# Kernel optimization log

Measured on AMD Instinct MI355X. Metric: run time of the kernel, lower is better.

Reference implementation:

```python
import jax, jax.numpy as jnp
import numpy as np

B, S, EMB, H = 4, 1024, 1024, 16
HD = EMB // H          # head_dim = 64
MAXP = 512             # RelativePositionalEncoder default max_position


def setup_inputs() -> dict:
    key = jax.random.key(0)
    ks = jax.random.split(key, 13)
    s = 1.0 / np.sqrt(EMB)  # xavier-ish scale keeps softmax logits sane
    return {
        "query": jax.random.normal(ks[0], (B, S, EMB), jnp.float32),
        "key": jax.random.normal(ks[1], (B, S, EMB), jnp.float32),
        "value": jax.random.normal(ks[2], (B, S, EMB), jnp.float32),
        "Wq": jax.random.normal(ks[3], (EMB, EMB), jnp.float32) * s,
        "bq": jnp.zeros((EMB,), jnp.float32),
        "Wk": jax.random.normal(ks[4], (EMB, EMB), jnp.float32) * s,
        "bk": jnp.zeros((EMB,), jnp.float32),
        "Wv": jax.random.normal(ks[5], (EMB, EMB), jnp.float32) * s,
        "bv": jnp.zeros((EMB,), jnp.float32),
        "Wo": jax.random.normal(ks[6], (EMB, EMB), jnp.float32) * s,
        "bo": jnp.zeros((EMB,), jnp.float32),
        "rel_k": jax.random.normal(ks[7], (2 * MAXP + 1, HD), jnp.float32) * 0.05,
        "rel_v": jax.random.normal(ks[8], (2 * MAXP + 1, HD), jnp.float32) * 0.05,
    }


def _split_heads(x):
    # [B,S,E] -> [B,S,H,HD] -> [B,H,S,HD] -> [B*H,S,HD]
    return x.reshape(B, S, H, HD).transpose(0, 2, 1, 3).reshape(B * H, S, HD)


def reference(query, key, value, Wq, bq, Wk, bk, Wv, bv, Wo, bo, rel_k, rel_v):
    scale = jnp.sqrt(jnp.asarray(HD, query.dtype))
    q = _split_heads(query @ Wq + bq)
    k = _split_heads(key @ Wk + bk)
    v = _split_heads(value @ Wv + bv)
    # relative position lookup tables: [Sq, Sk, HD]
    rp = jnp.clip(jnp.arange(S)[None, :] - jnp.arange(S)[:, None], -MAXP, MAXP) + MAXP
    a_key = rel_k[rp]
    a_value = rel_v[rp]
    qk = jnp.einsum('bqd,bkd->bqk', q, k)              # [B*H,S,S]
    rel_qk = jnp.einsum('bqd,qkd->bqk', q, a_key)      # relative score term
    attn = jax.nn.softmax((qk + rel_qk) / scale, axis=-1)
    out = jnp.einsum('bqk,bkd->bqd', attn, v) + jnp.einsum('bqk,qkd->bqd', attn, a_value)
    # faithful to original's view(num_heads, batch, -1, head_dim) then concat reshape
    out = out.reshape(H, B, S, HD).transpose(0, 2, 1, 3).reshape(B, S, H * HD)
    out = out @ Wo + bo
    return (out, attn)
```

## Files before the change

kernel.cpp:

```cpp
#include <hip/hip_runtime.h>


using s16x8 = __attribute__((ext_vector_type(8))) short;
using f32x4 = __attribute__((ext_vector_type(4))) float;

#define MFMA16 __builtin_amdgcn_mfma_f32_16x16x32_bf16

__device__ __forceinline__ float bf2f(unsigned short u) {
  union { unsigned int u; float f; } v; v.u = ((unsigned int)u) << 16; return v.f;
}
__device__ __forceinline__ unsigned short f2bf(float f) {
  union { float f; unsigned int u; } v; v.f = f;
  unsigned int r = (v.u + 0x7FFFu + ((v.u >> 16) & 1u)) >> 16;
  return (unsigned short)r;
}

__global__ void k_cvt_bf16(const float* __restrict__ in, unsigned short* __restrict__ out, int n) {
  int i = (blockIdx.x * 256 + threadIdx.x) * 8;
  if (i >= n) return;
  float4 a = *(const float4*)(in + i);
  float4 b = *(const float4*)(in + i + 4);
  s16x8 o;
  o[0] = (short)f2bf(a.x); o[1] = (short)f2bf(a.y); o[2] = (short)f2bf(a.z); o[3] = (short)f2bf(a.w);
  o[4] = (short)f2bf(b.x); o[5] = (short)f2bf(b.y); o[6] = (short)f2bf(b.z); o[7] = (short)f2bf(b.w);
  *(s16x8*)(out + i) = o;
}

__global__ void k_tr1024(const float* __restrict__ W, unsigned short* __restrict__ Wt) {
  __shared__ float t[32][33];
  int tx = threadIdx.x, ty = threadIdx.y;
  int n0 = blockIdx.x * 32, k0 = blockIdx.y * 32;
#pragma unroll
  for (int r = 0; r < 4; ++r)
    t[ty * 4 + r][tx] = W[(size_t)(k0 + ty * 4 + r) * 1024 + n0 + tx];
  __syncthreads();
#pragma unroll
  for (int r = 0; r < 4; ++r)
    Wt[(size_t)(n0 + ty * 4 + r) * 1024 + k0 + tx] = f2bf(t[tx][ty * 4 + r]);
}

__global__ void k_relprep(const float* __restrict__ rk, const float* __restrict__ rv,
                          unsigned short* __restrict__ relkb, unsigned short* __restrict__ rvTb) {
  int b = blockIdx.x;
  if (b < 33) {
    int i = (b * 256 + threadIdx.x) * 8;
    if (i < 65600) {
      float4 a = *(const float4*)(rk + i);
      float4 c = *(const float4*)(rk + i + 4);
      s16x8 o;
      o[0] = (short)f2bf(a.x); o[1] = (short)f2bf(a.y); o[2] = (short)f2bf(a.z); o[3] = (short)f2bf(a.w);
      o[4] = (short)f2bf(c.x); o[5] = (short)f2bf(c.y); o[6] = (short)f2bf(c.z); o[7] = (short)f2bf(c.w);
      *(s16x8*)(relkb + i) = o;
    }
  } else {
    int i = (b - 33) * 256 + threadIdx.x;
    if (i < 65600) {
      int p = i >> 6, d = i & 63;
      rvTb[d * 1040 + p] = f2bf(rv[i]);
    }
  }
}

__global__ __launch_bounds__(256)
void k_trV(const unsigned short* __restrict__ v, unsigned short* __restrict__ vt) {
  __shared__ unsigned short T[64][72];
  const int tid = threadIdx.x;
  const int bh = blockIdx.x >> 4;
  const int s0 = (blockIdx.x & 15) << 6;
  const int r = tid >> 2, cb = (tid & 3) << 4;
  const unsigned short* src = v + ((size_t)bh << 16) + (size_t)(s0 + r) * 64 + cb;
  *(s16x8*)&T[r][cb] = *(const s16x8*)src;
  *(s16x8*)&T[r][cb + 8] = *(const s16x8*)(src + 8);
  __syncthreads();
  unsigned short* dst = vt + ((size_t)bh << 16) + (size_t)r * 1024 + s0 + cb;
  s16x8 o0, o1;
#pragma unroll
  for (int e = 0; e < 8; ++e) o0[e] = T[cb + e][r];
#pragma unroll
  for (int e = 0; e < 8; ++e) o1[e] = T[cb + 8 + e][r];
  *(s16x8*)dst = o0;
  *(s16x8*)(dst + 8) = o1;
}

template <int MODE>
__global__ __launch_bounds__(256, 2)
void k_gemm(const unsigned short* __restrict__ A, const unsigned short* __restrict__ BT,
            const float* __restrict__ bias, void* __restrict__ Cout) {
  __shared__ alignas(16) unsigned short aT[2][4096];
  __shared__ alignas(16) unsigned short bT[2][2048];
  const int tid = threadIdx.x;
  const int lane = tid & 63;
  const int l15 = lane & 15, lhi = lane >> 4;
  const int w = tid >> 6;
  const int wr = w * 32;
  const int brow = blockIdx.y * 128, bcol = blockIdx.x * 64;
  f32x4 acc[2][4] = {};

#define STAGE(buf, kt) do {                                                              \
    int k0s = (kt) * 32;                                                                 \
    {                                                                                    \
      int c = tid;                                                                       \
      int row = c >> 2, k8 = (c & 3) * 8;                                                \
      __builtin_amdgcn_global_load_lds(                                                  \
        (const __attribute__((address_space(1))) void*)(A + (size_t)(brow + row) * 1024 + k0s + k8), \
        (__attribute__((address_space(3))) void*)(&aT[buf][c * 8]), 16, 0, 0);           \
      __builtin_amdgcn_global_load_lds(                                                  \
        (const __attribute__((address_space(1))) void*)(BT + (size_t)(bcol + row) * 1024 + k0s + k8),\
        (__attribute__((address_space(3))) void*)(&bT[buf][c * 8]), 16, 0, 0);           \
    }                                                                                    \
    {                                                                                    \
      int c = tid + 256;                                                                 \
      int row = c >> 2, k8 = (c & 3) * 8;                                                \
      __builtin_amdgcn_global_load_lds(                                                  \
        (const __attribute__((address_space(1))) void*)(A + (size_t)(brow + row) * 1024 + k0s + k8), \
        (__attribute__((address_space(3))) void*)(&aT[buf][c * 8]), 16, 0, 0);           \
    }                                                                                    \
  } while (0)

  int cur = 0;
  STAGE(0, 0);
  for (int kt = 0; kt < 32; ++kt) {
    __syncthreads();
    if (kt + 1 < 32) STAGE(cur ^ 1, kt + 1);
    s16x8 af[2], bfv[4];
#pragma unroll
    for (int m = 0; m < 2; ++m)
      af[m] = *(const s16x8*)&aT[cur][(wr + m * 16 + l15) * 32 + lhi * 8];
#pragma unroll
    for (int n = 0; n < 4; ++n)
      bfv[n] = *(const s16x8*)&bT[cur][(n * 16 + l15) * 32 + lhi * 8];
#pragma unroll
    for (int m = 0; m < 2; ++m)
#pragma unroll
      for (int n = 0; n < 4; ++n)
        acc[m][n] = MFMA16(af[m], bfv[n], acc[m][n], 0, 0, 0);
    __syncthreads();
    cur ^= 1;
  }
#undef STAGE

#pragma unroll
  for (int m = 0; m < 2; ++m) {
#pragma unroll
    for (int n = 0; n < 4; ++n) {
      int col = bcol + n * 16 + l15;
      float bs = bias[col];
#pragma unroll
      for (int j = 0; j < 4; ++j) {
        int r = brow + wr + m * 16 + lhi * 4 + j;
        float v = acc[m][n][j] + bs;
        if (MODE == 0) {
          int b = r >> 10, s = r & 1023, h = col >> 6, d = col & 63;
          ((unsigned short*)Cout)[(((size_t)((b << 4) + h) * 1024 + s) << 6) + d] = f2bf(v);
        } else {
          ((float*)Cout)[(size_t)r * 1024 + col] = v;
        }
      }
    }
  }
}

#define RPW 1032
#define PWP 520

__global__ __launch_bounds__(256, 3)
void k_attn(const unsigned short* __restrict__ qb, const unsigned short* __restrict__ kbm,
            const unsigned short* __restrict__ vT, const unsigned short* __restrict__ relk,
            const unsigned short* __restrict__ rvT, float* __restrict__ attn_out,
            unsigned short* __restrict__ xscr) {
  __shared__ alignas(16) unsigned short pbuf[16 * RPW];
  __shared__ alignas(16) unsigned short TbPw[16 * PWP];
  __shared__ float red[4][16];
  __shared__ float izS[16], plS[16], phS[16];
  __shared__ unsigned short bndS[32];

  const int tid = threadIdx.x;
  const int lane = tid & 63;
  const int w = tid >> 6;
  const int l15 = lane & 15, lhi = lane >> 4;
  const int orig = ((blockIdx.x & 7) << 9) | (blockIdx.x >> 3);
  const int bh = orig >> 6;
  const int q0 = (orig & 63) << 4;

  const unsigned short* Qh = qb + ((size_t)bh << 16);
  const unsigned short* Kh = kbm + ((size_t)bh << 16);
  const unsigned short* Vth = vT + ((size_t)bh << 16);

  const unsigned short* qp = Qh + (size_t)(q0 + l15) * 64 + lhi * 8;
  s16x8 qa0 = *(const s16x8*)qp;
  s16x8 qa1 = *(const s16x8*)(qp + 32);

  {
    int sel = (l15 == 1) ? 1024 : 0;
    const unsigned short* rp = relk + (size_t)sel * 64 + lhi * 8;
    s16x8 rb0 = *(const s16x8*)rp;
    s16x8 rb1 = *(const s16x8*)(rp + 32);
    f32x4 d = {0.f, 0.f, 0.f, 0.f};
    d = MFMA16(qa0, rb0, d, 0, 0, 0);
    d = MFMA16(qa1, rb1, d, 0, 0, 0);
    if (l15 < 2) {
#pragma unroll
      for (int j = 0; j < 4; ++j) bndS[l15 * 16 + lhi * 4 + j] = f2bf(d[j]);
    }
  }

  float zp = 0.f;
  for (int half = 0; half < 2; ++half) {
    const int khalf = half << 9;
    __syncthreads();

    for (int i = tid; i < 16 * 64; i += 256) {
      int row = i >> 6, c8 = (i & 63) << 3;
      int fl = q0 + row - khalf - 512;
      unsigned short vlo = bndS[row], vhi = bndS[16 + row];
      s16x8 o;
#pragma unroll
      for (int e = 0; e < 8; ++e) o[e] = (short)((c8 + e < fl) ? vlo : vhi);
      *(s16x8*)&TbPw[row * PWP + c8] = o;
    }
    __syncthreads();

    {
      int pmin = khalf - q0 + 497;
      int PT0 = (pmin < 0 ? 0 : pmin) & ~15;
      int PT1 = khalf - q0 + 1023; if (PT1 > 1024) PT1 = 1024;
      for (int pt = PT0 + w * 16; pt <= PT1; pt += 64) {
        int pr = pt + l15; if (pr > 1024) pr = 1024;
        const unsigned short* rp = relk + (size_t)pr * 64 + lhi * 8;
        s16x8 rf0 = *(const s16x8*)rp;
        s16x8 rf1 = *(const s16x8*)(rp + 32);
        f32x4 d = {0.f, 0.f, 0.f, 0.f};
        d = MFMA16(qa0, rf0, d, 0, 0, 0);
        d = MFMA16(qa1, rf1, d, 0, 0, 0);
#pragma unroll
        for (int j = 0; j < 4; ++j) {
          int qi = lhi * 4 + j;
          int p = pt + l15;
          int u = p - khalf + q0 + qi - 512;
          if (p <= 1024 && u >= 0 && u < 512) TbPw[qi * PWP + u] = f2bf(d[j]);
        }
      }
    }
    __syncthreads();

    for (int n = 0; n < 8; ++n) {
      const int ktile = khalf + w * 16 + n * 64;
      const unsigned short* kp = Kh + (size_t)(ktile + l15) * 64 + lhi * 8;
      s16x8 kf0 = *(const s16x8*)kp;
      s16x8 kf1 = *(const s16x8*)(kp + 32);
      f32x4 c = {0.f, 0.f, 0.f, 0.f};
      __builtin_amdgcn_s_setprio(1);
      c = MFMA16(kf0, qa0, c, 0, 0, 0);
      c = MFMA16(kf1, qa1, c, 0, 0, 0);
      __builtin_amdgcn_s_setprio(0);
      uint2 tv = *(const uint2*)&TbPw[l15 * PWP + (ktile - khalf) + lhi * 4];
      float t0 = bf2f((unsigned short)(tv.x & 0xFFFF));
      float t1 = bf2f((unsigned short)(tv.x >> 16));
      float t2 = bf2f((unsigned short)(tv.y & 0xFFFF));
      float t3 = bf2f((unsigned short)(tv.y >> 16));
      float e0 = __expf((c[0] + t0) * 0.125f);
      float e1 = __expf((c[1] + t1) * 0.125f);
      float e2 = __expf((c[2] + t2) * 0.125f);
      float e3 = __expf((c[3] + t3) * 0.125f);
      zp += (e0 + e1) + (e2 + e3);
      uint2 pk;
      pk.x = (unsigned int)f2bf(e0) | ((unsigned int)f2bf(e1) << 16);
      pk.y = (unsigned int)f2bf(e2) | ((unsigned int)f2bf(e3) << 16);
      *(uint2*)&pbuf[l15 * RPW + ktile + lhi * 4] = pk;
    }
  }

  zp += __shfl_xor(zp, 16, 64);
  zp += __shfl_xor(zp, 32, 64);
  if (lane < 16) red[w][lane] = zp;
  __syncthreads();
  if (tid < 16)
    izS[tid] = 1.0f / (red[0][tid] + red[1][tid] + red[2][tid] + red[3][tid]);

  {
    const int qi = tid >> 4, tq = tid & 15;
    const int qa = q0 + qi;
    int lo, hi;
    const bool isPh = (qa < 512);
    if (isPh) { lo = qa + 512; hi = 1024; }
    else      { lo = 0;        hi = qa - 511; }
    float s = 0.f;
    const unsigned short* srow = pbuf + qi * RPW;
    const int kb0 = lo & ~7;
    for (int k8 = kb0 + tq * 8; k8 < hi; k8 += 128) {
      s16x8 v8 = *(const s16x8*)&srow[k8];
#pragma unroll
      for (int e = 0; e < 8; ++e) {
        int k = k8 + e;
        s += (k >= lo && k < hi) ? bf2f((unsigned short)v8[e]) : 0.f;
      }
    }
#pragma unroll
    for (int off = 1; off < 16; off <<= 1) s += __shfl_xor(s, off, 64);
    if (tq == 0) { plS[qi] = isPh ? 0.f : s; phS[qi] = isPh ? s : 0.f; }
  }
  __syncthreads();

  {
    float* ao = attn_out + ((size_t)bh << 20) + ((size_t)q0 << 10);
#pragma unroll
    for (int n = 0; n < 8; ++n) {
      int row = (tid >> 7) + n * 2;
      int c8 = (tid & 127) << 3;
      float iz = izS[row];
      s16x8 p8 = *(const s16x8*)&pbuf[row * RPW + c8];
      f32x4 o0, o1;
      o0[0] = bf2f((unsigned short)p8[0]) * iz; o0[1] = bf2f((unsigned short)p8[1]) * iz;
      o0[2] = bf2f((unsigned short)p8[2]) * iz; o0[3] = bf2f((unsigned short)p8[3]) * iz;
      o1[0] = bf2f((unsigned short)p8[4]) * iz; o1[1] = bf2f((unsigned short)p8[5]) * iz;
      o1[2] = bf2f((unsigned short)p8[6]) * iz; o1[3] = bf2f((unsigned short)p8[7]) * iz;
      __builtin_nontemporal_store(o0, (f32x4*)(ao + (row << 10) + c8));
      __builtin_nontemporal_store(o1, (f32x4*)(ao + (row << 10) + c8 + 4));
    }
  }

  f32x4 acc = {0.f, 0.f, 0.f, 0.f};
  const int d0w = w << 4;
  const unsigned short* vrow = Vth + (size_t)(d0w + l15) * 1024 + lhi * 8;
#pragma unroll 8
  for (int kc = 0; kc < 1024; kc += 32) {
    s16x8 pa = *(const s16x8*)&pbuf[l15 * RPW + kc + lhi * 8];
    s16x8 vf = *(const s16x8*)(vrow + kc);
    acc = MFMA16(pa, vf, acc, 0, 0, 0);
  }

  const unsigned short* rrow = rvT + (size_t)(d0w + l15) * 1040 + lhi * 8;
  {
    const int sqi = tid >> 4, stq = tid & 15;
    const int ssh = sqi & 7, shs = ssh >> 1;
    const bool sodd = (ssh & 1) != 0;
    unsigned short* drow = TbPw + sqi * PWP;
    const unsigned short* srow = pbuf + sqi * RPW;
    for (int ph = 0; ph < 2; ++ph) {
      __syncthreads();
      const int base = q0 + sqi + (ph ? 0 : -512);
      for (int t = stq; t < 64; t += 16) {
        const int kw0 = base + t * 8;
        s16x8 o;
        if (kw0 >= 0 && kw0 + 8 <= 1024) {
          const int A = kw0 - ssh;
          union { s16x8 v; unsigned int u[4]; } a0, a1, ov;
          a0.v = *(const s16x8*)&srow[A];
          a1.v = *(const s16x8*)&srow[A + 8];
          unsigned int wd[8];
#pragma unroll
          for (int j2 = 0; j2 < 4; ++j2) { wd[j2] = a0.u[j2]; wd[4 + j2] = a1.u[j2]; }
          unsigned int v7[7];
#pragma unroll
          for (int j2 = 0; j2 < 7; ++j2) {
            unsigned int sf = (wd[j2] >> 16) | (wd[j2 + 1] << 16);
            v7[j2] = sodd ? sf : wd[j2];
          }
#pragma unroll
          for (int j2 = 0; j2 < 4; ++j2) {
            unsigned int t0 = (shs & 1) ? v7[j2 + 1] : v7[j2];
            unsigned int t1 = (shs & 1) ? v7[j2 + 3] : v7[j2 + 2];
            ov.u[j2] = (shs & 2) ? t1 : t0;
          }
          o = ov.v;
        } else if (kw0 + 8 <= 0 || kw0 >= 1024) {
          o = (s16x8){0, 0, 0, 0, 0, 0, 0, 0};
        } else {
#pragma unroll
          for (int e = 0; e < 8; ++e) {
            int k = kw0 + e;
            int kc2 = k < 0 ? 0 : (k > 1023 ? 1023 : k);
            unsigned short vv = srow[kc2];
            o[e] = (k >= 0 && k < 1024) ? (short)vv : (short)0;
          }
        }
        *(s16x8*)&drow[t * 8] = o;
        if (ph == 0 && t == 0) drow[0] = f2bf(plS[sqi]);
      }
      __syncthreads();
#pragma unroll 8
      for (int kc = 0; kc < 512; kc += 32) {
        s16x8 pa = *(const s16x8*)&TbPw[l15 * PWP + kc + lhi * 8];
        s16x8 rb = *(const s16x8*)(rrow + (ph << 9) + kc);
        acc = MFMA16(pa, rb, acc, 0, 0, 0);
      }
    }
  }

  float rv1024 = bf2f(rvT[(size_t)(d0w + l15) * 1040 + 1024]);
  const size_t fb = ((size_t)(bh >> 2) << 18) + ((size_t)(bh & 3) << 6);
#pragma unroll
  for (int j = 0; j < 4; ++j) {
    int qi = lhi * 4 + j;
    float v = (acc[j] + phS[qi] * rv1024) * izS[qi];
    xscr[fb + ((size_t)(q0 + qi) << 8) + d0w + l15] = f2bf(v);
  }
}

extern "C" void kernel_launch(void* const* d_in, const int* in_sizes, int n_in,
                              void* d_out, int out_size, void* d_ws, size_t ws_size,
                              hipStream_t stream) {
  (void)in_sizes; (void)n_in; (void)out_size; (void)ws_size;
  const float* query = (const float*)d_in[0];
  const float* key   = (const float*)d_in[1];
  const float* value = (const float*)d_in[2];
  const float* Wq = (const float*)d_in[3];
  const float* bq = (const float*)d_in[4];
  const float* Wk = (const float*)d_in[5];
  const float* bk = (const float*)d_in[6];
  const float* Wv = (const float*)d_in[7];
  const float* bv = (const float*)d_in[8];
  const float* Wo = (const float*)d_in[9];
  const float* bo = (const float*)d_in[10];
  const float* rel_k = (const float*)d_in[11];
  const float* rel_v = (const float*)d_in[12];

  char* ws = (char*)d_ws;
  const size_t MB = 1024 * 1024;
  unsigned short* qb    = (unsigned short*)(ws);
  unsigned short* kbuf  = (unsigned short*)(ws + 8 * MB);
  unsigned short* vbuf  = (unsigned short*)(ws + 16 * MB);
  unsigned short* tmp16 = (unsigned short*)(ws + 24 * MB);
  unsigned short* wt    = (unsigned short*)(ws + 32 * MB);
  unsigned short* relkb = (unsigned short*)(ws + 34 * MB);
  unsigned short* rvTb  = (unsigned short*)(ws + 34 * MB + 512 * 1024);
  unsigned short* vTb   = tmp16;
  unsigned short* xscr  = vbuf;

  float* out0 = (float*)d_out;
  float* attn_out = out0 + 4194304;

  dim3 trb(32, 8), trg(32, 32);
  dim3 gg(16, 32);

  k_relprep<<<290, 256, 0, stream>>>(rel_k, rel_v, relkb, rvTb);

  k_cvt_bf16<<<2048, 256, 0, stream>>>(query, tmp16, 4194304);
  k_tr1024<<<trg, trb, 0, stream>>>(Wq, wt);
  k_gemm<0><<<gg, 256, 0, stream>>>(tmp16, wt, bq, qb);

  k_cvt_bf16<<<2048, 256, 0, stream>>>(key, tmp16, 4194304);
  k_tr1024<<<trg, trb, 0, stream>>>(Wk, wt);
  k_gemm<0><<<gg, 256, 0, stream>>>(tmp16, wt, bk, kbuf);

  k_cvt_bf16<<<2048, 256, 0, stream>>>(value, tmp16, 4194304);
  k_tr1024<<<trg, trb, 0, stream>>>(Wv, wt);
  k_gemm<0><<<gg, 256, 0, stream>>>(tmp16, wt, bv, vbuf);

  k_trV<<<1024, 256, 0, stream>>>(vbuf, vTb);
  k_tr1024<<<trg, trb, 0, stream>>>(Wo, wt);

  k_attn<<<4096, 256, 0, stream>>>(qb, kbuf, vTb, relkb, rvTb, attn_out, xscr);

  k_gemm<1><<<gg, 256, 0, stream>>>(xscr, wt, bo, out0);
}
```

Baseline: 368.6 us.

## Double attention block to 512 threads with split-K PV and LDS reduction

Raises k_attn from 4 to 8 waves per block. The score, rel-key and row-sum loops are re-strided across the extra waves, and the PV and rel-value MFMA loops are split over K so each pair of waves covers half the keys. The two partial accumulators are combined through shared memory before the output is written. This aims to give each block more latency hiding and parallelism, at the cost of extra barriers, an LDS reduction step, and launch bounds (512, 6) that tighten the per-thread register budget.

```diff
diff --git a/kernel.cpp b/kernel.cpp
--- a/kernel.cpp
+++ b/kernel.cpp
@@ -163,14 +163,14 @@
 #define RPW 1032
 #define PWP 520
 
-__global__ __launch_bounds__(256, 3)
+__global__ __launch_bounds__(512, 6)
 void k_attn(const unsigned short* __restrict__ qb, const unsigned short* __restrict__ kbm,
             const unsigned short* __restrict__ vT, const unsigned short* __restrict__ relk,
             const unsigned short* __restrict__ rvT, float* __restrict__ attn_out,
             unsigned short* __restrict__ xscr) {
   __shared__ alignas(16) unsigned short pbuf[16 * RPW];
   __shared__ alignas(16) unsigned short TbPw[16 * PWP];
-  __shared__ float red[4][16];
+  __shared__ float red[8][16];
   __shared__ float izS[16], plS[16], phS[16];
   __shared__ unsigned short bndS[32];
 
@@ -190,7 +190,7 @@
   s16x8 qa0 = *(const s16x8*)qp;
   s16x8 qa1 = *(const s16x8*)(qp + 32);
 
-  {
+  if (w == 0) {
     int sel = (l15 == 1) ? 1024 : 0;
     const unsigned short* rp = relk + (size_t)sel * 64 + lhi * 8;
     s16x8 rb0 = *(const s16x8*)rp;
@@ -209,7 +209,7 @@
     const int khalf = half << 9;
     __syncthreads();
 
-    for (int i = tid; i < 16 * 64; i += 256) {
+    for (int i = tid; i < 16 * 64; i += 512) {
       int row = i >> 6, c8 = (i & 63) << 3;
       int fl = q0 + row - khalf - 512;
       unsigned short vlo = bndS[row], vhi = bndS[16 + row];
@@ -224,7 +224,7 @@
       int pmin = khalf - q0 + 497;
       int PT0 = (pmin < 0 ? 0 : pmin) & ~15;
       int PT1 = khalf - q0 + 1023; if (PT1 > 1024) PT1 = 1024;
-      for (int pt = PT0 + w * 16; pt <= PT1; pt += 64) {
+      for (int pt = PT0 + w * 16; pt <= PT1; pt += 128) {
         int pr = pt + l15; if (pr > 1024) pr = 1024;
         const unsigned short* rp = relk + (size_t)pr * 64 + lhi * 8;
         s16x8 rf0 = *(const s16x8*)rp;
@@ -243,8 +243,8 @@
     }
     __syncthreads();
 
-    for (int n = 0; n < 8; ++n) {
-      const int ktile = khalf + w * 16 + n * 64;
+    for (int n = 0; n < 4; ++n) {
+      const int ktile = khalf + w * 16 + n * 128;
       const unsigned short* kp = Kh + (size_t)(ktile + l15) * 64 + lhi * 8;
       s16x8 kf0 = *(const s16x8*)kp;
       s16x8 kf1 = *(const s16x8*)(kp + 32);
@@ -274,11 +274,15 @@
   zp += __shfl_xor(zp, 32, 64);
   if (lane < 16) red[w][lane] = zp;
   __syncthreads();
-  if (tid < 16)
-    izS[tid] = 1.0f / (red[0][tid] + red[1][tid] + red[2][tid] + red[3][tid]);
+  if (tid < 16) {
+    float s = 0.f;
+#pragma unroll
+    for (int ww = 0; ww < 8; ++ww) s += red[ww][tid];
+    izS[tid] = 1.0f / s;
+  }
 
   {
-    const int qi = tid >> 4, tq = tid & 15;
+    const int qi = tid >> 5, tq = tid & 31;
     const int qa = q0 + qi;
     int lo, hi;
     const bool isPh = (qa < 512);
@@ -287,7 +291,7 @@
     float s = 0.f;
     const unsigned short* srow = pbuf + qi * RPW;
     const int kb0 = lo & ~7;
-    for (int k8 = kb0 + tq * 8; k8 < hi; k8 += 128) {
+    for (int k8 = kb0 + tq * 8; k8 < hi; k8 += 256) {
       s16x8 v8 = *(const s16x8*)&srow[k8];
 #pragma unroll
       for (int e = 0; e < 8; ++e) {
@@ -296,7 +300,7 @@
       }
     }
 #pragma unroll
-    for (int off = 1; off < 16; off <<= 1) s += __shfl_xor(s, off, 64);
+    for (int off = 1; off < 32; off <<= 1) s += __shfl_xor(s, off, 64);
     if (tq == 0) { plS[qi] = isPh ? 0.f : s; phS[qi] = isPh ? s : 0.f; }
   }
   __syncthreads();
@@ -304,9 +308,9 @@
   {
     float* ao = attn_out + ((size_t)bh << 20) + ((size_t)q0 << 10);
 #pragma unroll
-    for (int n = 0; n < 8; ++n) {
-      int row = (tid >> 7) + n * 2;
-      int c8 = (tid & 127) << 3;
+    for (int n = 0; n < 4; ++n) {
+      int idx = n * 512 + tid;
+      int row = idx >> 7, c8 = (idx & 127) << 3;
       float iz = izS[row];
       s16x8 p8 = *(const s16x8*)&pbuf[row * RPW + c8];
       f32x4 o0, o1;
@@ -320,26 +324,28 @@
   }
 
   f32x4 acc = {0.f, 0.f, 0.f, 0.f};
-  const int d0w = w << 4;
-  const unsigned short* vrow = Vth + (size_t)(d0w + l15) * 1024 + lhi * 8;
+  const int d0 = (w >> 1) << 4;
+  const int kbase = (w & 1) << 9;
+  const unsigned short* vrow = Vth + (size_t)(d0 + l15) * 1024 + lhi * 8;
 #pragma unroll 8
-  for (int kc = 0; kc < 1024; kc += 32) {
+  for (int kc = kbase; kc < kbase + 512; kc += 32) {
     s16x8 pa = *(const s16x8*)&pbuf[l15 * RPW + kc + lhi * 8];
     s16x8 vf = *(const s16x8*)(vrow + kc);
     acc = MFMA16(pa, vf, acc, 0, 0, 0);
   }
 
-  const unsigned short* rrow = rvT + (size_t)(d0w + l15) * 1040 + lhi * 8;
+  const unsigned short* rrow = rvT + (size_t)(d0 + l15) * 1040 + lhi * 8;
   {
-    const int sqi = tid >> 4, stq = tid & 15;
+    const int sqi = tid >> 5, stq = tid & 31;
     const int ssh = sqi & 7, shs = ssh >> 1;
     const bool sodd = (ssh & 1) != 0;
     unsigned short* drow = TbPw + sqi * PWP;
     const unsigned short* srow = pbuf + sqi * RPW;
+    const int kq = (w & 1) << 8;
     for (int ph = 0; ph < 2; ++ph) {
       __syncthreads();
       const int base = q0 + sqi + (ph ? 0 : -512);
-      for (int t = stq; t < 64; t += 16) {
+      for (int t = stq; t < 64; t += 32) {
         const int kw0 = base + t * 8;
         s16x8 o;
         if (kw0 >= 0 && kw0 + 8 <= 1024) {
@@ -379,7 +385,7 @@
       }
       __syncthreads();
 #pragma unroll 8
-      for (int kc = 0; kc < 512; kc += 32) {
+      for (int kc = kq; kc < kq + 256; kc += 32) {
         s16x8 pa = *(const s16x8*)&TbPw[l15 * PWP + kc + lhi * 8];
         s16x8 rb = *(const s16x8*)(rrow + (ph << 9) + kc);
         acc = MFMA16(pa, rb, acc, 0, 0, 0);
@@ -387,13 +393,23 @@
     }
   }
 
-  float rv1024 = bf2f(rvT[(size_t)(d0w + l15) * 1040 + 1024]);
-  const size_t fb = ((size_t)(bh >> 2) << 18) + ((size_t)(bh & 3) << 6);
-#pragma unroll
-  for (int j = 0; j < 4; ++j) {
-    int qi = lhi * 4 + j;
-    float v = (acc[j] + phS[qi] * rv1024) * izS[qi];
-    xscr[fb + ((size_t)(q0 + qi) << 8) + d0w + l15] = f2bf(v);
+  __syncthreads();
+  float* fscr = (float*)TbPw;
+  if (w & 1) {
+    f32x4* dst = (f32x4*)&fscr[(((w >> 1) << 6) | lane) << 2];
+    *dst = acc;
+  }
+  __syncthreads();
+  if (!(w & 1)) {
+    f32x4 other = *(const f32x4*)&fscr[(((w >> 1) << 6) | lane) << 2];
+    float rv1024 = bf2f(rvT[(size_t)(d0 + l15) * 1040 + 1024]);
+    const size_t fb = ((size_t)(bh >> 2) << 18) + ((size_t)(bh & 3) << 6);
+#pragma unroll
+    for (int j = 0; j < 4; ++j) {
+      int qi = lhi * 4 + j;
+      float v = (acc[j] + other[j] + phS[qi] * rv1024) * izS[qi];
+      xscr[fb + ((size_t)(q0 + qi) << 8) + d0 + l15] = f2bf(v);
+    }
   }
 }
 
@@ -450,7 +466,7 @@
   k_trV<<<1024, 256, 0, stream>>>(vbuf, vTb);
   k_tr1024<<<trg, trb, 0, stream>>>(Wo, wt);
 
-  k_attn<<<4096, 256, 0, stream>>>(qb, kbuf, vTb, relkb, rvTb, attn_out, xscr);
+  k_attn<<<4096, 512, 0, stream>>>(qb, kbuf, vTb, relkb, rvTb, attn_out, xscr);
 
   k_gemm<1><<<gg, 256, 0, stream>>>(xscr, wt, bo, out0);
 }
```

Result: slower. 402.1 us (+9.1%).
